# Kernel tuning notes

Hardware: AMD Instinct MI355X
Metric: run time of the kernel (lower is better)

The kernel has to match this reference:

```python
import jax, jax.numpy as jnp
import numpy as np

N_NODES = 20000
N_EDGES = 160000
N_GRAPHS = 64
IN_DIM = 1304  # 1280 + 24
NEG_SLOPE = 0.2


def gat_conv(x, src, dst, W, a_src, a_dst, b, heads, out_ch):
    """PyG-style GATConv (source_to_target flow, self loops already appended).
    x: [N, in], W: [in, heads*out], a_src/a_dst: [heads, out], b: [heads*out].
    Returns [N, heads*out] (concat=True)."""
    N = x.shape[0]
    h = (x @ W).reshape(N, heads, out_ch)                 # [N, H, C]
    e_src = jnp.sum(h * a_src[None], axis=-1)             # [N, H]
    e_dst = jnp.sum(h * a_dst[None], axis=-1)             # [N, H]
    e = jax.nn.leaky_relu(e_src[src] + e_dst[dst], NEG_SLOPE)  # [E, H]
    # softmax over incoming edges of each destination node
    e_max = jax.ops.segment_max(e, dst, num_segments=N)   # [N, H]
    e_exp = jnp.exp(e - e_max[dst])
    denom = jax.ops.segment_sum(e_exp, dst, num_segments=N)
    alpha = e_exp / (denom[dst] + 1e-16)                  # [E, H]
    msg = h[src] * alpha[:, :, None]                      # [E, H, C]
    out = jax.ops.segment_sum(msg, dst, num_segments=N)   # [N, H, C]
    return out.reshape(N, heads * out_ch) + b


def setup_inputs() -> dict:
    key = jax.random.key(0)
    ks = jax.random.split(key, 20)
    x = jax.random.normal(ks[0], (N_NODES, IN_DIM), dtype=jnp.float32)
    edge_index = jax.random.randint(ks[1], (2, N_EDGES), 0, N_NODES, dtype=jnp.int32)
    phy = jax.random.normal(ks[2], (N_GRAPHS, 188), dtype=jnp.float32)
    batch = jnp.sort(jax.random.randint(ks[3], (N_NODES,), 0, N_GRAPHS, dtype=jnp.int32))

    def glorot(k, shape):
        fan_in, fan_out = shape[0], shape[-1]
        lim = jnp.sqrt(6.0 / (fan_in + fan_out))
        return jax.random.uniform(k, shape, jnp.float32, -lim, lim)

    params = {
        # conv1: GATConv(1304, 256, heads=3)
        "W1": glorot(ks[4], (IN_DIM, 3 * 256)),
        "a_src1": glorot(ks[5], (3, 256)) * 0.1,
        "a_dst1": glorot(ks[6], (3, 256)) * 0.1,
        "b1": jnp.zeros((3 * 256,), jnp.float32),
        # conv2: GATConv(768, 256, heads=1)
        "W2": glorot(ks[7], (3 * 256, 256)),
        "a_src2": glorot(ks[8], (1, 256)) * 0.1,
        "a_dst2": glorot(ks[9], (1, 256)) * 0.1,
        "b2": jnp.zeros((256,), jnp.float32),
        # fc1
        "fc1_w1": glorot(ks[10], (188, 128)), "fc1_b1": jnp.zeros((128,), jnp.float32),
        "fc1_w2": glorot(ks[11], (128, 128)), "fc1_b2": jnp.zeros((128,), jnp.float32),
        # fc2
        "fc2_w1": glorot(ks[12], (256 + 128, 192)), "fc2_b1": jnp.zeros((192,), jnp.float32),
        "fc2_w2": glorot(ks[13], (192, 2)), "fc2_b2": jnp.zeros((2,), jnp.float32),
    }
    return {"x": x, "edge_index": edge_index, "phy": phy, "batch": batch, **params}


def reference(x, edge_index, phy, batch,
              W1, a_src1, a_dst1, b1,
              W2, a_src2, a_dst2, b2,
              fc1_w1, fc1_b1, fc1_w2, fc1_b2,
              fc2_w1, fc2_b1, fc2_w2, fc2_b2):
    N = x.shape[0]
    # add self loops (PyG GATConv default)
    loops = jnp.arange(N, dtype=edge_index.dtype)
    src = jnp.concatenate([edge_index[0], loops])
    dst = jnp.concatenate([edge_index[1], loops])

    h = gat_conv(x, src, dst, W1, a_src1, a_dst1, b1, heads=3, out_ch=256)
    h = jax.nn.relu(h)  # dropout is identity at inference
    h = gat_conv(h, src, dst, W2, a_src2, a_dst2, b2, heads=1, out_ch=256)

    # global mean pool per graph
    sums = jax.ops.segment_sum(h, batch, num_segments=N_GRAPHS)        # [B, 256]
    cnts = jax.ops.segment_sum(jnp.ones((N,), h.dtype), batch, num_segments=N_GRAPHS)
    pooled = sums / jnp.maximum(cnts, 1.0)[:, None]

    mid = jax.nn.relu(phy @ fc1_w1 + fc1_b1)
    mid = jax.nn.relu(mid @ fc1_w2 + fc1_b2)

    z = jnp.concatenate([pooled, mid], axis=1)                          # [B, 384]
    z = jax.nn.relu(z @ fc2_w1 + fc2_b1)
    logits = z @ fc2_w2 + fc2_b2
    return jax.nn.softmax(logits, axis=1)
```

## Files before the change

kernel.cpp:

```cpp
#include <hip/hip_runtime.h>
#include <hip/hip_bf16.h>
#include <math.h>

#define NN    20000
#define MP1   20224
#define NP    20096
#define E0    160000
#define EL    180000
#define NG    64
#define INDIM 1304
#define K1P   1344
#define GNT   21
#define GNX   3
#define GMB   79
#define NWG1  (GMB * GNX)
#define FB    19
#define NEG_SLOPE 0.2f
#define NSB   20
#define PCH   32

#define ZB    80
#define XB    13272
#define WB    4800

typedef __bf16 bf16x8 __attribute__((ext_vector_type(8)));
typedef __bf16 bf16x4 __attribute__((ext_vector_type(4)));
typedef float  f32x4  __attribute__((ext_vector_type(4)));

__device__ __forceinline__ void gload16(const void* g, void* l) {
    __builtin_amdgcn_global_load_lds(
        (const __attribute__((address_space(1))) void*)g,
        (__attribute__((address_space(3))) void*)l, 16, 0, 0);
}

#define BAR()  { __builtin_amdgcn_s_barrier(); asm volatile("" ::: "memory"); }
#define VMW(n) { asm volatile("s_waitcnt vmcnt(" #n ")" ::: "memory"); __builtin_amdgcn_sched_barrier(0); }

__global__ __launch_bounds__(256)
void init_kernel(uint4* __restrict__ zreg, int n16,
                 const float* __restrict__ X, __hip_bfloat16* __restrict__ Xb,
                 const float* __restrict__ W1, const float* __restrict__ W2,
                 __hip_bfloat16* __restrict__ w1t, __hip_bfloat16* __restrict__ w2t) {
    const int b = blockIdx.x, t = threadIdx.x;
    if (b < ZB) {
        int i = b * 256 + t;
        if (i < n16) zreg[i] = (uint4){0u, 0u, 0u, 0u};
        return;
    }
    if (b < ZB + XB) {
        int idx = (b - ZB) * 256 + t;
        const int nb = K1P / 8;
        int row = idx / nb;
        int cb = (idx - row * nb) * 8;
        union { __hip_bfloat16 h[8]; float4 f4; } u;
        if (row < NN && cb + 8 <= INDIM) {
            const float4* p = (const float4*)(X + (size_t)row * INDIM + cb);
            float4 u0 = p[0], u1 = p[1];
            u.h[0] = __float2bfloat16(u0.x); u.h[1] = __float2bfloat16(u0.y);
            u.h[2] = __float2bfloat16(u0.z); u.h[3] = __float2bfloat16(u0.w);
            u.h[4] = __float2bfloat16(u1.x); u.h[5] = __float2bfloat16(u1.y);
            u.h[6] = __float2bfloat16(u1.z); u.h[7] = __float2bfloat16(u1.w);
        } else {
#pragma unroll
            for (int e = 0; e < 8; e++) {
                float f = (row < NN && cb + e < INDIM) ? X[(size_t)row * INDIM + cb + e] : 0.f;
                u.h[e] = __float2bfloat16(f);
            }
        }
        *(float4*)(Xb + (size_t)row * K1P + cb) = u.f4;
        return;
    }
    {
        int idx = (b - ZB - XB) * 256 + t;
        const int n1 = 768 * K1P;
        if (idx < n1) {
            int n = idx / K1P, k = idx - n * K1P;
            float f = (k < INDIM) ? W1[(size_t)k * 768 + n] : 0.f;
            w1t[idx] = __float2bfloat16(f);
        } else {
            int i2 = idx - n1;
            if (i2 < 256 * 768) {
                int n = i2 / 768, k = i2 - n * 768;
                w2t[i2] = __float2bfloat16(W2[(size_t)k * 256 + n]);
            }
        }
    }
}

__device__ __forceinline__ void stA(const __hip_bfloat16* __restrict__ A, int bm, int kt, int mh,
                                    char* abuf, int w, int l) {
#pragma unroll
    for (int u = 0; u < 2; u++) {
        int rl = (w << 3) + (l >> 3);
        int lrow = u * 128 + mh * 64 + rl;
        int skb = ((l & 7) << 4) ^ ((rl & 7) << 4);
        const char* g = (const char*)(A + (size_t)(bm + lrow) * K1P + kt * 64) + skb;
        gload16(g, abuf + (u * 128 + mh * 64) * 128 + (w << 10));
    }
}

__device__ __forceinline__ void stB(const __hip_bfloat16* __restrict__ Bt, int bn, int kt, int nh,
                                    char* bbuf, int w, int l) {
#pragma unroll
    for (int u = 0; u < 2; u++) {
        int c = u * 2 + (w >> 2);
        int row0 = c * 64 + nh * 32;
        int rl = ((w & 3) << 3) + (l >> 3);
        int skb = ((l & 7) << 4) ^ ((rl & 7) << 4);
        const char* g = (const char*)(Bt + (size_t)(bn + row0 + rl) * K1P + kt * 64) + skb;
        gload16(g, bbuf + row0 * 128 + ((w & 3) << 10));
    }
}

__global__ __launch_bounds__(512)
void gemm256(const __hip_bfloat16* __restrict__ A,
             const __hip_bfloat16* __restrict__ Bt,
             __hip_bfloat16* __restrict__ C,
             const float* __restrict__ a_src, const float* __restrict__ a_dst,
             float* __restrict__ esrc, float* __restrict__ edst, int M,
             const int* __restrict__ ei, const int* __restrict__ off,
             int* __restrict__ cur, int* __restrict__ csr) {
    __shared__ char lds[65536];
    const int t = threadIdx.x;

    if (blockIdx.x >= NWG1) {
        for (int e = (blockIdx.x - NWG1) * 512 + t; e < EL; e += FB * 512) {
            int d = (e < E0) ? ei[E0 + e] : (e - E0);
            int s = (e < E0) ? ei[e] : (e - E0);
            int pos = off[d] + atomicAdd(&cur[d], 1);
            csr[pos] = s;
        }
        return;
    }

    const int w = t >> 6, l = t & 63;
    const int wm = w >> 2, wn = w & 3;
    const int fr = l & 15, fq = l >> 4;
    const int amask = (fr & 7) << 4;

    const int nwg = NWG1;
    const int q8 = nwg >> 3, r8 = nwg & 7;
    const int xcd = blockIdx.x & 7, sub = blockIdx.x >> 3;
    const int logical = (xcd < r8 ? xcd * (q8 + 1) : r8 * (q8 + 1) + (xcd - r8) * q8) + sub;
    const int bm = (logical / GNX) * 256;
    const int bn = (logical % GNX) * 256;

    f32x4 acc[8][4];
#pragma unroll
    for (int i = 0; i < 8; i++)
#pragma unroll
        for (int j = 0; j < 4; j++) acc[i][j] = (f32x4){0.f, 0.f, 0.f, 0.f};

    char* Ab = lds;
    char* Bb = lds + 32768;

    stA(A, bm, 0, 0, Ab, w, l);
    stB(Bt, bn, 0, 0, Bb, w, l);
    stB(Bt, bn, 0, 1, Bb, w, l);
    stA(A, bm, 0, 1, Ab, w, l);

    for (int kt = 0; kt < GNT; kt++) {
        const bool nl = (kt + 1 < GNT);
        bf16x8 a_c[4][2], b_c0[2][2], b_c1[2][2];

        VMW(4);
        BAR();
#pragma unroll
        for (int im = 0; im < 4; im++)
#pragma unroll
            for (int kk = 0; kk < 2; kk++)
                a_c[im][kk] = *(const bf16x8*)(Ab + (wm * 128 + im * 16 + fr) * 128 + ((kk * 64 + fq * 16) ^ amask));
#pragma unroll
        for (int jn = 0; jn < 2; jn++)
#pragma unroll
            for (int kk = 0; kk < 2; kk++)
                b_c0[jn][kk] = *(const bf16x8*)(Bb + (wn * 64 + jn * 16 + fr) * 128 + ((kk * 64 + fq * 16) ^ amask));
        if (nl) stA(A, bm, kt + 1, 0, Ab, w, l);
        __builtin_amdgcn_s_setprio(1);
#pragma unroll
        for (int im = 0; im < 4; im++)
#pragma unroll
            for (int jn = 0; jn < 2; jn++)
#pragma unroll
                for (int kk = 0; kk < 2; kk++)
                    acc[im][jn] = __builtin_amdgcn_mfma_f32_16x16x32_bf16(a_c[im][kk], b_c0[jn][kk], acc[im][jn], 0, 0, 0);
        __builtin_amdgcn_s_setprio(0);

        if (nl) { VMW(4); } else { VMW(2); }
        BAR();
#pragma unroll
        for (int jn = 0; jn < 2; jn++)
#pragma unroll
            for (int kk = 0; kk < 2; kk++)
                b_c1[jn][kk] = *(const bf16x8*)(Bb + (wn * 64 + 32 + jn * 16 + fr) * 128 + ((kk * 64 + fq * 16) ^ amask));
        if (nl) stB(Bt, bn, kt + 1, 0, Bb, w, l);
        __builtin_amdgcn_s_setprio(1);
#pragma unroll
        for (int im = 0; im < 4; im++)
#pragma unroll
            for (int jn = 0; jn < 2; jn++)
#pragma unroll
                for (int kk = 0; kk < 2; kk++)
                    acc[im][2 + jn] = __builtin_amdgcn_mfma_f32_16x16x32_bf16(a_c[im][kk], b_c1[jn][kk], acc[im][2 + jn], 0, 0, 0);
        __builtin_amdgcn_s_setprio(0);

        if (nl) { VMW(4); } else { VMW(0); }
        BAR();
#pragma unroll
        for (int im = 0; im < 4; im++)
#pragma unroll
            for (int kk = 0; kk < 2; kk++)
                a_c[im][kk] = *(const bf16x8*)(Ab + (wm * 128 + 64 + im * 16 + fr) * 128 + ((kk * 64 + fq * 16) ^ amask));
        if (nl) stB(Bt, bn, kt + 1, 1, Bb, w, l);
        __builtin_amdgcn_s_setprio(1);
#pragma unroll
        for (int im = 0; im < 4; im++)
#pragma unroll
            for (int jn = 0; jn < 2; jn++)
#pragma unroll
                for (int kk = 0; kk < 2; kk++)
                    acc[4 + im][jn] = __builtin_amdgcn_mfma_f32_16x16x32_bf16(a_c[im][kk], b_c0[jn][kk], acc[4 + im][jn], 0, 0, 0);
        __builtin_amdgcn_s_setprio(0);

        if (nl) stA(A, bm, kt + 1, 1, Ab, w, l);
        __builtin_amdgcn_s_setprio(1);
#pragma unroll
        for (int im = 0; im < 4; im++)
#pragma unroll
            for (int jn = 0; jn < 2; jn++)
#pragma unroll
                for (int kk = 0; kk < 2; kk++)
                    acc[4 + im][2 + jn] = __builtin_amdgcn_mfma_f32_16x16x32_bf16(a_c[im][kk], b_c1[jn][kk], acc[4 + im][2 + jn], 0, 0, 0);
        __builtin_amdgcn_s_setprio(0);
    }

#pragma unroll
    for (int i = 0; i < 8; i++)
#pragma unroll
        for (int j = 0; j < 4; j++)
#pragma unroll
            for (int r = 0; r < 4; r++) {
                int row = bm + wm * 128 + i * 16 + fq * 4 + r;
                int col = bn + wn * 64 + j * 16 + fr;
                if (row < M) C[(size_t)row * 768 + col] = __float2bfloat16(acc[i][j][r]);
            }

    const int head = bn >> 8;
    float asv[4], adv[4];
#pragma unroll
    for (int j = 0; j < 4; j++) {
        asv[j] = a_src[head * 256 + wn * 64 + j * 16 + fr];
        adv[j] = a_dst[head * 256 + wn * 64 + j * 16 + fr];
    }
    __syncthreads();
    float* eb = (float*)lds;
#pragma unroll
    for (int i = 0; i < 8; i++) {
#pragma unroll
        for (int r = 0; r < 4; r++) {
            float ps = 0.f, pd = 0.f;
#pragma unroll
            for (int j = 0; j < 4; j++) { ps += acc[i][j][r] * asv[j]; pd += acc[i][j][r] * adv[j]; }
#pragma unroll
            for (int o = 8; o >= 1; o >>= 1) { ps += __shfl_xor(ps, o, 64); pd += __shfl_xor(pd, o, 64); }
            if (fr == 0) {
                int rowl = wm * 128 + i * 16 + fq * 4 + r;
                eb[(rowl * 4 + wn) * 2 + 0] = ps;
                eb[(rowl * 4 + wn) * 2 + 1] = pd;
            }
        }
    }
    __syncthreads();
    if (t < 256) {
        int row = bm + t;
        if (row < M) {
            float s = eb[t * 8 + 0] + eb[t * 8 + 2] + eb[t * 8 + 4] + eb[t * 8 + 6];
            float d = eb[t * 8 + 1] + eb[t * 8 + 3] + eb[t * 8 + 5] + eb[t * 8 + 7];
            esrc[row * 3 + head] = s;
            edst[row * 3 + head] = d;
        }
    }
}

__global__ __launch_bounds__(256)
void gemm2_fused(const __hip_bfloat16* __restrict__ A,
                 const __hip_bfloat16* __restrict__ Bt,
                 __hip_bfloat16* __restrict__ C,
                 const float* __restrict__ a_src2, const float* __restrict__ a_dst2,
                 float* __restrict__ esrc, float* __restrict__ edst,
                 int M, int N, int K, int NX) {
    __shared__ __hip_bfloat16 As[2][128 * 32];
    __shared__ __hip_bfloat16 Bs[2][128 * 32];
    const int t = threadIdx.x;
    const int w = t >> 6;
    const int l = t & 63;

    const int nwg = gridDim.x;
    const int q = nwg >> 3, r = nwg & 7;
    const int xcd = blockIdx.x & 7, idx = blockIdx.x >> 3;
    const int logical = (xcd < r ? xcd * (q + 1) : r * (q + 1) + (xcd - r) * q) + idx;
    const int bm = (logical / NX) * 128;
    const int bn = (logical % NX) * 128;

    const int wm = (w >> 1) * 64;
    const int wn = (w & 1) * 64;

    f32x4 acc[4][4];
#pragma unroll
    for (int i = 0; i < 4; i++)
#pragma unroll
        for (int j = 0; j < 4; j++) acc[i][j] = (f32x4){0.f, 0.f, 0.f, 0.f};

    const int sr = t >> 2;
    const int sc = (t & 3) * 8;
    const __hip_bfloat16* a0 = A  + (size_t)(bm + sr)      * K + sc;
    const __hip_bfloat16* a1 = A  + (size_t)(bm + 64 + sr) * K + sc;
    const __hip_bfloat16* b0 = Bt + (size_t)(bn + sr)      * K + sc;
    const __hip_bfloat16* b1 = Bt + (size_t)(bn + 64 + sr) * K + sc;

    const int fr = l & 15;
    const int fq = l >> 4;
    const int NT = K / 32;

    auto stage = [&](int k0, int b) {
        char* asb = (char*)&As[b][0];
        char* bsb = (char*)&Bs[b][0];
        gload16(a0 + k0, asb + w * 1024);
        gload16(a1 + k0, asb + 4096 + w * 1024);
        gload16(b0 + k0, bsb + w * 1024);
        gload16(b1 + k0, bsb + 4096 + w * 1024);
    };

    stage(0, 0);
    __syncthreads();

    for (int kt = 0; kt < NT; kt++) {
        const int cb = kt & 1;
        if (kt + 1 < NT) stage((kt + 1) * 32, cb ^ 1);
        bf16x8 av[4], bv[4];
#pragma unroll
        for (int i = 0; i < 4; i++)
            av[i] = *(const bf16x8*)&As[cb][(wm + i * 16 + fr) * 32 + fq * 8];
#pragma unroll
        for (int j = 0; j < 4; j++)
            bv[j] = *(const bf16x8*)&Bs[cb][(wn + j * 16 + fr) * 32 + fq * 8];
#pragma unroll
        for (int i = 0; i < 4; i++)
#pragma unroll
            for (int j = 0; j < 4; j++)
                acc[i][j] = __builtin_amdgcn_mfma_f32_16x16x32_bf16(av[i], bv[j], acc[i][j], 0, 0, 0);
        __syncthreads();
    }

#pragma unroll
    for (int i = 0; i < 4; i++) {
#pragma unroll
        for (int j = 0; j < 4; j++) {
#pragma unroll
            for (int r2 = 0; r2 < 4; r2++) {
                int row = bm + wm + i * 16 + fq * 4 + r2;
                int col = bn + wn + j * 16 + fr;
                if (row < M) C[(size_t)row * N + col] = __float2bfloat16(acc[i][j][r2]);
            }
        }
    }

    float asv[4], adv[4];
#pragma unroll
    for (int j = 0; j < 4; j++) {
        asv[j] = a_src2[bn + wn + j * 16 + fr];
        adv[j] = a_dst2[bn + wn + j * 16 + fr];
    }
    __syncthreads();
    float* eb = (float*)&As[0][0];
#pragma unroll
    for (int i = 0; i < 4; i++) {
#pragma unroll
        for (int r2 = 0; r2 < 4; r2++) {
            float ps = 0.f, pd = 0.f;
#pragma unroll
            for (int j = 0; j < 4; j++) { ps += acc[i][j][r2] * asv[j]; pd += acc[i][j][r2] * adv[j]; }
#pragma unroll
            for (int o = 8; o >= 1; o >>= 1) { ps += __shfl_xor(ps, o, 64); pd += __shfl_xor(pd, o, 64); }
            if (fr == 0) {
                int rowl = wm + i * 16 + fq * 4 + r2;
                int wnIdx = wn >> 6;
                eb[(rowl * 2 + wnIdx) * 2 + 0] = ps;
                eb[(rowl * 2 + wnIdx) * 2 + 1] = pd;
            }
        }
    }
    __syncthreads();
    if (t < 128) {
        int row = bm + t;
        if (row < M) {
            atomicAdd(&esrc[row], eb[t * 4 + 0] + eb[t * 4 + 2]);
            atomicAdd(&edst[row], eb[t * 4 + 1] + eb[t * 4 + 3]);
        }
    }
}

__global__ void hist_kernel(const int* __restrict__ ei, int* __restrict__ deg) {
    int e = blockIdx.x * 256 + threadIdx.x;
    if (e >= EL) return;
    int d = (e < E0) ? ei[E0 + e] : (e - E0);
    atomicAdd(&deg[d], 1);
}

__global__ __launch_bounds__(1024)
void scan_blk(const int* __restrict__ deg, int* __restrict__ off, int* __restrict__ bsum) {
    __shared__ int wsum[16];
    const int b = blockIdx.x, t = threadIdx.x, lane = t & 63, wv = t >> 6;
    const int i = b * 1024 + t;
    int v = (i < NN) ? deg[i] : 0;
    int x = v;
#pragma unroll
    for (int o = 1; o < 64; o <<= 1) {
        int y = __shfl_up(x, o, 64);
        if (lane >= o) x += y;
    }
    if (lane == 63) wsum[wv] = x;
    __syncthreads();
    if (wv == 0 && lane < 16) {
        int s = wsum[lane];
#pragma unroll
        for (int o = 1; o < 16; o <<= 1) {
            int y = __shfl_up(s, o, 64);
            if (lane >= o) s += y;
        }
        wsum[lane] = s;
    }
    __syncthreads();
    int woff = (wv == 0) ? 0 : wsum[wv - 1];
    if (i < NN) off[i + 1] = woff + x;
    if (t == 1023) bsum[b] = wsum[15];
}

__global__ __launch_bounds__(1024)
void scan_add(int* __restrict__ off, const int* __restrict__ bsum) {
    __shared__ int boffs[NSB];
    const int b = blockIdx.x, t = threadIdx.x;
    if (t < 64) {
        int lane = t;
        int v = (lane < NSB) ? bsum[lane] : 0;
        int x = v;
#pragma unroll
        for (int o = 1; o < 64; o <<= 1) {
            int y = __shfl_up(x, o, 64);
            if (lane >= o) x += y;
        }
        if (lane < NSB) boffs[lane] = x - v;
    }
    __syncthreads();
    const int i = b * 1024 + t;
    if (i < NN) off[i + 1] += boffs[b];
    if (b == 0 && t == 0) off[0] = 0;
}

template<int H, bool RELU, typename OutT>
__global__ __launch_bounds__(256)
void gat_aggregate(const __hip_bfloat16* __restrict__ hfeat,
                   const float* __restrict__ esrc,
                   const float* __restrict__ edst,
                   const int* __restrict__ off, const int* __restrict__ csr,
                   const float* __restrict__ bias,
                   OutT* __restrict__ out, int N) {
    const int wv = threadIdx.x >> 6, lane = threadIdx.x & 63;
    const int pair = blockIdx.x * 4 + wv;
    if (pair >= N * H) return;
    const int n = pair / H;
    const int h = pair - n * H;
    const int beg = off[n];
    const int deg = off[n + 1] - beg;

    const float ed = edst[n * H + h];
    float m = -INFINITY, den = 0.f;
    f32x4 acc = (f32x4){0.f, 0.f, 0.f, 0.f};

    for (int base = 0; base < deg; base += 64) {
        const int i = base + lane;
        int s = 0;
        float lg = -INFINITY;
        if (i < deg) {
            s = csr[beg + i];
            float v = esrc[s * H + h] + ed;
            lg = (v >= 0.f) ? v : NEG_SLOPE * v;
        }
        float cm = lg;
#pragma unroll
        for (int o = 1; o < 64; o <<= 1)
            cm = fmaxf(cm, __shfl_xor(cm, o, 64));
        float nm = fmaxf(m, cm);
        float sc = expf(m - nm);
        den *= sc;
#pragma unroll
        for (int e = 0; e < 4; e++) acc[e] *= sc;
        m = nm;
        float wgt = (i < deg) ? expf(lg - m) : 0.f;
        den += wgt;
        const int cnt = min(64, deg - base);
        for (int j = 0; j < cnt; j++) {
            int sj = __shfl(s, j, 64);
            float wj = __shfl(wgt, j, 64);
            bf16x4 hv = *(const bf16x4*)(hfeat + (size_t)sj * (H * 256) + h * 256 + 4 * lane);
#pragma unroll
            for (int e = 0; e < 4; e++) acc[e] += wj * (float)hv[e];
        }
    }
#pragma unroll
    for (int o = 1; o < 64; o <<= 1) den += __shfl_xor(den, o, 64);

    float inv = 1.f / (den + 1e-16f);
    if constexpr (sizeof(OutT) == 2) {
        bf16x4 r;
#pragma unroll
        for (int e = 0; e < 4; e++) {
            float f = acc[e] * inv + bias[h * 256 + 4 * lane + e];
            if (RELU) f = fmaxf(f, 0.f);
            r[e] = (__bf16)f;
        }
        *(bf16x4*)((__hip_bfloat16*)out + (size_t)n * (H * 256) + h * 256 + 4 * lane) = r;
    } else {
        float4 r;
        float* rp = &r.x;
#pragma unroll
        for (int e = 0; e < 4; e++) {
            float f = acc[e] * inv + bias[h * 256 + 4 * lane + e];
            if (RELU) f = fmaxf(f, 0.f);
            rp[e] = f;
        }
        *(float4*)((float*)out + (size_t)n * (H * 256) + h * 256 + 4 * lane) = r;
    }
}

__device__ __forceinline__ int lower_bound_batch(const int* __restrict__ batch, int key) {
    int lo = 0, hi = NN;
    while (lo < hi) {
        int mid = (lo + hi) >> 1;
        if (batch[mid] < key) lo = mid + 1; else hi = mid;
    }
    return lo;
}

__global__ __launch_bounds__(256)
void pool_partial(const __hip_bfloat16* __restrict__ out2, const int* __restrict__ batch,
                  float* __restrict__ partial, float* __restrict__ cnts) {
    const int g = blockIdx.x, c = blockIdx.y, t = threadIdx.x;
    const int s = lower_bound_batch(batch, g);
    const int e = lower_bound_batch(batch, g + 1);
    float a0 = 0.f, a1 = 0.f, a2 = 0.f, a3 = 0.f;
    int n = s + c;
    for (; n + 3 * PCH < e; n += 4 * PCH) {
        float v0 = __bfloat162float(out2[(size_t)n * 256 + t]);
        float v1 = __bfloat162float(out2[(size_t)(n + PCH) * 256 + t]);
        float v2 = __bfloat162float(out2[(size_t)(n + 2 * PCH) * 256 + t]);
        float v3 = __bfloat162float(out2[(size_t)(n + 3 * PCH) * 256 + t]);
        a0 += v0; a1 += v1; a2 += v2; a3 += v3;
    }
    for (; n < e; n += PCH) a0 += __bfloat162float(out2[(size_t)n * 256 + t]);
    partial[((size_t)g * PCH + c) * 256 + t] = a0 + a1 + a2 + a3;
    if (t == 0 && c == 0) cnts[g] = (float)(e - s);
}

__global__ __launch_bounds__(256)
void head_kernel(const float* __restrict__ partial, const float* __restrict__ cnts,
                 const float* __restrict__ phy,
                 const float* __restrict__ w11, const float* __restrict__ b11,
                 const float* __restrict__ w12, const float* __restrict__ b12,
                 const float* __restrict__ w21, const float* __restrict__ b21,
                 const float* __restrict__ w22, const float* __restrict__ b22,
                 float* __restrict__ out) {
    int g = blockIdx.x, t = threadIdx.x;
    __shared__ float ph[188];
    __shared__ float z[384];
    __shared__ float mid[128];
    __shared__ float t1[192];
    __shared__ float lg[2];
    if (t < 188) ph[t] = phy[g * 188 + t];
    {
        float s = 0.f;
#pragma unroll
        for (int c = 0; c < PCH; c++) s += partial[((size_t)g * PCH + c) * 256 + t];
        z[t] = s / fmaxf(cnts[g], 1.0f);
    }
    __syncthreads();
    if (t < 128) {
        float sm = b11[t];
        for (int k = 0; k < 188; k++) sm += ph[k] * w11[k * 128 + t];
        mid[t] = fmaxf(sm, 0.f);
    }
    __syncthreads();
    if (t < 128) {
        float sm = b12[t];
        for (int k = 0; k < 128; k++) sm += mid[k] * w12[k * 128 + t];
        z[256 + t] = fmaxf(sm, 0.f);
    }
    __syncthreads();
    if (t < 192) {
        float sm = b21[t];
        for (int k = 0; k < 384; k++) sm += z[k] * w21[k * 192 + t];
        t1[t] = fmaxf(sm, 0.f);
    }
    __syncthreads();
    if (t < 2) {
        float sm = b22[t];
        for (int k = 0; k < 192; k++) sm += t1[k] * w22[k * 2 + t];
        lg[t] = sm;
    }
    __syncthreads();
    if (t == 0) {
        float mx = fmaxf(lg[0], lg[1]);
        float e0 = expf(lg[0] - mx), e1 = expf(lg[1] - mx);
        float d = e0 + e1;
        out[g * 2 + 0] = e0 / d;
        out[g * 2 + 1] = e1 / d;
    }
}

extern "C" void kernel_launch(void* const* d_in, const int* in_sizes, int n_in,
                              void* d_out, int out_size, void* d_ws, size_t ws_size,
                              hipStream_t stream) {
    const float* x       = (const float*)d_in[0];
    const int*   ei      = (const int*)  d_in[1];
    const float* phy     = (const float*)d_in[2];
    const int*   batch   = (const int*)  d_in[3];
    const float* W1      = (const float*)d_in[4];
    const float* a_src1  = (const float*)d_in[5];
    const float* a_dst1  = (const float*)d_in[6];
    const float* b1      = (const float*)d_in[7];
    const float* W2      = (const float*)d_in[8];
    const float* a_src2  = (const float*)d_in[9];
    const float* a_dst2  = (const float*)d_in[10];
    const float* b2      = (const float*)d_in[11];
    const float* fc1_w1  = (const float*)d_in[12];
    const float* fc1_b1  = (const float*)d_in[13];
    const float* fc1_w2  = (const float*)d_in[14];
    const float* fc1_b2  = (const float*)d_in[15];
    const float* fc2_w1  = (const float*)d_in[16];
    const float* fc2_b1  = (const float*)d_in[17];
    const float* fc2_w2  = (const float*)d_in[18];
    const float* fc2_b2  = (const float*)d_in[19];
    float* out = (float*)d_out;

    char* base = (char*)d_ws;
    size_t o = 0;
    auto alloc = [&](size_t bytes) { size_t r = o; o += (bytes + 255) & ~255ULL; return r; };

    size_t o_xb   = alloc((size_t)MP1 * K1P * 2);
    size_t o_w1t  = alloc((size_t)768 * K1P * 2);
    size_t o_w2t  = alloc((size_t)256 * 768 * 2);
    size_t o_h1b  = alloc((size_t)NP * 768 * 2);
    size_t o_hob  = alloc((size_t)NP * 768 * 2);
    size_t o_es1  = alloc((size_t)NN * 3 * 4);
    size_t o_ed1  = alloc((size_t)NN * 3 * 4);
    size_t o_es2  = alloc((size_t)NN * 4);
    size_t o_ed2  = alloc((size_t)NN * 4);
    size_t o_deg  = alloc((size_t)(NN + 1) * 4);
    size_t o_cur  = alloc((size_t)NN * 4);
    size_t o_zend = o;
    size_t o_off  = alloc((size_t)(NN + 1) * 4);
    size_t o_csr  = alloc((size_t)EL * 4);
    size_t o_bsum = alloc((size_t)NSB * 4);
    size_t o_part = alloc((size_t)NG * PCH * 256 * 4);
    size_t o_cnts = alloc((size_t)NG * 4);

    __hip_bfloat16* xb   = (__hip_bfloat16*)(base + o_xb);
    __hip_bfloat16* w1t  = (__hip_bfloat16*)(base + o_w1t);
    __hip_bfloat16* w2t  = (__hip_bfloat16*)(base + o_w2t);
    __hip_bfloat16* h1b  = (__hip_bfloat16*)(base + o_h1b);
    __hip_bfloat16* hob  = (__hip_bfloat16*)(base + o_hob);
    __hip_bfloat16* h2b  = (__hip_bfloat16*)(base + o_xb);
    __hip_bfloat16* out2 = (__hip_bfloat16*)(base + o_xb + (size_t)24 * 1024 * 1024);
    float* es1   = (float*)(base + o_es1);
    float* ed1   = (float*)(base + o_ed1);
    float* es2   = (float*)(base + o_es2);
    float* ed2   = (float*)(base + o_ed2);
    int*   deg   = (int*)(base + o_deg);
    int*   cur   = (int*)(base + o_cur);
    int*   offs  = (int*)(base + o_off);
    int*   csr   = (int*)(base + o_csr);
    int*   bsum  = (int*)(base + o_bsum);
    float* part  = (float*)(base + o_part);
    float* cnts  = (float*)(base + o_cnts);

    {
        int n16 = (int)((o_zend - o_es2) / 16);
        init_kernel<<<ZB + XB + WB, 256, 0, stream>>>((uint4*)(base + o_es2), n16,
                                                      x, xb, W1, W2, w1t, w2t);
    }

    hist_kernel<<<(EL + 255) / 256, 256, 0, stream>>>(ei, deg);
    scan_blk<<<NSB, 1024, 0, stream>>>(deg, offs, bsum);
    scan_add<<<NSB, 1024, 0, stream>>>(offs, bsum);

    gemm256<<<NWG1 + FB, 512, 0, stream>>>(xb, w1t, h1b, a_src1, a_dst1, es1, ed1, NN,
                                           ei, offs, cur, csr);
    gat_aggregate<3, true, __hip_bfloat16><<<(NN * 3 + 3) / 4, 256, 0, stream>>>(h1b, es1, ed1, offs, csr, b1, hob, NN);

    gemm2_fused<<<2 * 157, 256, 0, stream>>>(hob, w2t, h2b, a_src2, a_dst2, es2, ed2, NN, 256, 768, 2);
    gat_aggregate<1, false, __hip_bfloat16><<<(NN + 3) / 4, 256, 0, stream>>>(h2b, es2, ed2, offs, csr, b2, out2, NN);

    pool_partial<<<dim3(NG, PCH), 256, 0, stream>>>(out2, batch, part, cnts);
    head_kernel<<<NG, 256, 0, stream>>>(part, cnts, phy,
                                        fc1_w1, fc1_b1, fc1_w2, fc1_b2,
                                        fc2_w1, fc2_b1, fc2_w2, fc2_b2, out);
}
```

Measured before the change: 230.3 us.

## Fuse fp32-to-bf16 conversion of X into GEMM A-tile loading

Drops the separate pass that converted X to a padded bf16 copy in init_kernel. The first GEMM now reads fp32 X directly into registers, converts to bf16 and writes swizzled tiles into LDS, with reworked vmcnt/lgkmcnt waits to keep the loads overlapped. This removes a full write and re-read of the converted matrix (about 54 MB of traffic). In exchange each A tile pulls twice the bytes from global memory, and the register staging can cost registers or weaken latency hiding in the main loop.

```diff
diff --git a/kernel.cpp b/kernel.cpp
--- a/kernel.cpp
+++ b/kernel.cpp
@@ -3,12 +3,12 @@
 #include <math.h>
 
 #define NN    20000
-#define MP1   20224
 #define NP    20096
 #define E0    160000
 #define EL    180000
 #define NG    64
 #define INDIM 1304
+#define NG8   (INDIM / 8)
 #define K1P   1344
 #define GNT   21
 #define GNX   3
@@ -20,7 +20,6 @@
 #define PCH   32
 
 #define ZB    80
-#define XB    13272
 #define WB    4800
 
 typedef __bf16 bf16x8 __attribute__((ext_vector_type(8)));
@@ -35,10 +34,10 @@
 
 #define BAR()  { __builtin_amdgcn_s_barrier(); asm volatile("" ::: "memory"); }
 #define VMW(n) { asm volatile("s_waitcnt vmcnt(" #n ")" ::: "memory"); __builtin_amdgcn_sched_barrier(0); }
+#define LGW()  { asm volatile("s_waitcnt lgkmcnt(0)" ::: "memory"); __builtin_amdgcn_sched_barrier(0); }
 
 __global__ __launch_bounds__(256)
 void init_kernel(uint4* __restrict__ zreg, int n16,
-                 const float* __restrict__ X, __hip_bfloat16* __restrict__ Xb,
                  const float* __restrict__ W1, const float* __restrict__ W2,
                  __hip_bfloat16* __restrict__ w1t, __hip_bfloat16* __restrict__ w2t) {
     const int b = blockIdx.x, t = threadIdx.x;
@@ -47,31 +46,8 @@
         if (i < n16) zreg[i] = (uint4){0u, 0u, 0u, 0u};
         return;
     }
-    if (b < ZB + XB) {
+    {
         int idx = (b - ZB) * 256 + t;
-        const int nb = K1P / 8;
-        int row = idx / nb;
-        int cb = (idx - row * nb) * 8;
-        union { __hip_bfloat16 h[8]; float4 f4; } u;
-        if (row < NN && cb + 8 <= INDIM) {
-            const float4* p = (const float4*)(X + (size_t)row * INDIM + cb);
-            float4 u0 = p[0], u1 = p[1];
-            u.h[0] = __float2bfloat16(u0.x); u.h[1] = __float2bfloat16(u0.y);
-            u.h[2] = __float2bfloat16(u0.z); u.h[3] = __float2bfloat16(u0.w);
-            u.h[4] = __float2bfloat16(u1.x); u.h[5] = __float2bfloat16(u1.y);
-            u.h[6] = __float2bfloat16(u1.z); u.h[7] = __float2bfloat16(u1.w);
-        } else {
-#pragma unroll
-            for (int e = 0; e < 8; e++) {
-                float f = (row < NN && cb + e < INDIM) ? X[(size_t)row * INDIM + cb + e] : 0.f;
-                u.h[e] = __float2bfloat16(f);
-            }
-        }
-        *(float4*)(Xb + (size_t)row * K1P + cb) = u.f4;
-        return;
-    }
-    {
-        int idx = (b - ZB - XB) * 256 + t;
         const int n1 = 768 * K1P;
         if (idx < n1) {
             int n = idx / K1P, k = idx - n * K1P;
@@ -87,15 +63,34 @@
     }
 }
 
-__device__ __forceinline__ void stA(const __hip_bfloat16* __restrict__ A, int bm, int kt, int mh,
-                                    char* abuf, int w, int l) {
+__device__ __forceinline__ void aLoad(const float* __restrict__ X, int bm, int kt, int mh,
+                                      int w, int l, float4 (&v)[2][2]) {
+    const int g8 = min(kt * 8 + (l & 7), NG8 - 1);
+    const int rl = (w << 3) + (l >> 3);
 #pragma unroll
     for (int u = 0; u < 2; u++) {
-        int rl = (w << 3) + (l >> 3);
         int lrow = u * 128 + mh * 64 + rl;
-        int skb = ((l & 7) << 4) ^ ((rl & 7) << 4);
-        const char* g = (const char*)(A + (size_t)(bm + lrow) * K1P + kt * 64) + skb;
-        gload16(g, abuf + (u * 128 + mh * 64) * 128 + (w << 10));
+        int row = min(bm + lrow, NN - 1);
+        const float4* p = (const float4*)(X + (size_t)row * INDIM + g8 * 8);
+        v[u][0] = p[0];
+        v[u][1] = p[1];
+    }
+}
+
+__device__ __forceinline__ void aWrite(char* abuf, int bm, int kt, int mh, int w, int l,
+                                       const float4 (&v)[2][2]) {
+    const bool cok = (kt * 8 + (l & 7)) < NG8;
+    const int rl = (w << 3) + (l >> 3);
+#pragma unroll
+    for (int u = 0; u < 2; u++) {
+        int lrow = u * 128 + mh * 64 + rl;
+        bool ok = cok && (bm + lrow < NN);
+        union { __hip_bfloat16 h[8]; bf16x8 vv; } uu;
+        const float* f = (const float*)&v[u][0];
+#pragma unroll
+        for (int e = 0; e < 8; e++) uu.h[e] = __float2bfloat16(ok ? f[e] : 0.f);
+        int byte = lrow * 128 + ((((l & 7) << 4)) ^ ((rl & 7) << 4));
+        *(bf16x8*)(abuf + byte) = uu.vv;
     }
 }
 
@@ -113,7 +108,7 @@
 }
 
 __global__ __launch_bounds__(512)
-void gemm256(const __hip_bfloat16* __restrict__ A,
+void gemm256(const float* __restrict__ X,
              const __hip_bfloat16* __restrict__ Bt,
              __hip_bfloat16* __restrict__ C,
              const float* __restrict__ a_src, const float* __restrict__ a_dst,
@@ -154,16 +149,21 @@
     char* Ab = lds;
     char* Bb = lds + 32768;
 
-    stA(A, bm, 0, 0, Ab, w, l);
+    float4 av0[2][2], av1[2][2];
+
+    aLoad(X, bm, 0, 0, w, l, av0);
+    aLoad(X, bm, 0, 1, w, l, av1);
     stB(Bt, bn, 0, 0, Bb, w, l);
     stB(Bt, bn, 0, 1, Bb, w, l);
-    stA(A, bm, 0, 1, Ab, w, l);
+    VMW(8); aWrite(Ab, bm, 0, 0, w, l, av0);
+    VMW(4); aWrite(Ab, bm, 0, 1, w, l, av1);
+    LGW();
 
     for (int kt = 0; kt < GNT; kt++) {
         const bool nl = (kt + 1 < GNT);
         bf16x8 a_c[4][2], b_c0[2][2], b_c1[2][2];
 
-        VMW(4);
+        if (kt == 0) { VMW(2); } else { VMW(6); }
         BAR();
 #pragma unroll
         for (int im = 0; im < 4; im++)
@@ -175,7 +175,9 @@
 #pragma unroll
             for (int kk = 0; kk < 2; kk++)
                 b_c0[jn][kk] = *(const bf16x8*)(Bb + (wn * 64 + jn * 16 + fr) * 128 + ((kk * 64 + fq * 16) ^ amask));
-        if (nl) stA(A, bm, kt + 1, 0, Ab, w, l);
+        if (nl) aLoad(X, bm, kt + 1, 0, w, l, av0);
+        if (nl) { VMW(4); } else { VMW(0); }
+        if (kt > 0) aWrite(Ab, bm, kt, 1, w, l, av1);
         __builtin_amdgcn_s_setprio(1);
 #pragma unroll
         for (int im = 0; im < 4; im++)
@@ -185,15 +187,19 @@
                 for (int kk = 0; kk < 2; kk++)
                     acc[im][jn] = __builtin_amdgcn_mfma_f32_16x16x32_bf16(a_c[im][kk], b_c0[jn][kk], acc[im][jn], 0, 0, 0);
         __builtin_amdgcn_s_setprio(0);
-
-        if (nl) { VMW(4); } else { VMW(2); }
+        LGW();
+
         BAR();
 #pragma unroll
         for (int jn = 0; jn < 2; jn++)
 #pragma unroll
             for (int kk = 0; kk < 2; kk++)
                 b_c1[jn][kk] = *(const bf16x8*)(Bb + (wn * 64 + 32 + jn * 16 + fr) * 128 + ((kk * 64 + fq * 16) ^ amask));
-        if (nl) stB(Bt, bn, kt + 1, 0, Bb, w, l);
+        if (nl) {
+            stB(Bt, bn, kt + 1, 0, Bb, w, l);
+            VMW(2);
+            aWrite(Ab, bm, kt + 1, 0, w, l, av0);
+        }
         __builtin_amdgcn_s_setprio(1);
 #pragma unroll
         for (int im = 0; im < 4; im++)
@@ -203,8 +209,8 @@
                 for (int kk = 0; kk < 2; kk++)
                     acc[im][2 + jn] = __builtin_amdgcn_mfma_f32_16x16x32_bf16(a_c[im][kk], b_c1[jn][kk], acc[im][2 + jn], 0, 0, 0);
         __builtin_amdgcn_s_setprio(0);
-
-        if (nl) { VMW(4); } else { VMW(0); }
+        LGW();
+
         BAR();
 #pragma unroll
         for (int im = 0; im < 4; im++)
@@ -222,7 +228,7 @@
                     acc[4 + im][jn] = __builtin_amdgcn_mfma_f32_16x16x32_bf16(a_c[im][kk], b_c0[jn][kk], acc[4 + im][jn], 0, 0, 0);
         __builtin_amdgcn_s_setprio(0);
 
-        if (nl) stA(A, bm, kt + 1, 1, Ab, w, l);
+        if (nl) aLoad(X, bm, kt + 1, 1, w, l, av1);
         __builtin_amdgcn_s_setprio(1);
 #pragma unroll
         for (int im = 0; im < 4; im++)
@@ -646,7 +652,7 @@
     size_t o = 0;
     auto alloc = [&](size_t bytes) { size_t r = o; o += (bytes + 255) & ~255ULL; return r; };
 
-    size_t o_xb   = alloc((size_t)MP1 * K1P * 2);
+    size_t o_scr  = alloc((size_t)48 * 1024 * 1024);
     size_t o_w1t  = alloc((size_t)768 * K1P * 2);
     size_t o_w2t  = alloc((size_t)256 * 768 * 2);
     size_t o_h1b  = alloc((size_t)NP * 768 * 2);
@@ -664,13 +670,12 @@
     size_t o_part = alloc((size_t)NG * PCH * 256 * 4);
     size_t o_cnts = alloc((size_t)NG * 4);
 
-    __hip_bfloat16* xb   = (__hip_bfloat16*)(base + o_xb);
     __hip_bfloat16* w1t  = (__hip_bfloat16*)(base + o_w1t);
     __hip_bfloat16* w2t  = (__hip_bfloat16*)(base + o_w2t);
     __hip_bfloat16* h1b  = (__hip_bfloat16*)(base + o_h1b);
     __hip_bfloat16* hob  = (__hip_bfloat16*)(base + o_hob);
-    __hip_bfloat16* h2b  = (__hip_bfloat16*)(base + o_xb);
-    __hip_bfloat16* out2 = (__hip_bfloat16*)(base + o_xb + (size_t)24 * 1024 * 1024);
+    __hip_bfloat16* h2b  = (__hip_bfloat16*)(base + o_scr);
+    __hip_bfloat16* out2 = (__hip_bfloat16*)(base + o_scr + (size_t)24 * 1024 * 1024);
     float* es1   = (float*)(base + o_es1);
     float* ed1   = (float*)(base + o_ed1);
     float* es2   = (float*)(base + o_es2);
@@ -685,15 +690,15 @@
 
     {
         int n16 = (int)((o_zend - o_es2) / 16);
-        init_kernel<<<ZB + XB + WB, 256, 0, stream>>>((uint4*)(base + o_es2), n16,
-                                                      x, xb, W1, W2, w1t, w2t);
+        init_kernel<<<ZB + WB, 256, 0, stream>>>((uint4*)(base + o_es2), n16,
+                                                 W1, W2, w1t, w2t);
     }
 
     hist_kernel<<<(EL + 255) / 256, 256, 0, stream>>>(ei, deg);
     scan_blk<<<NSB, 1024, 0, stream>>>(deg, offs, bsum);
     scan_add<<<NSB, 1024, 0, stream>>>(offs, bsum);
 
-    gemm256<<<NWG1 + FB, 512, 0, stream>>>(xb, w1t, h1b, a_src1, a_dst1, es1, ed1, NN,
+    gemm256<<<NWG1 + FB, 512, 0, stream>>>(x, w1t, h1b, a_src1, a_dst1, es1, ed1, NN,
                                            ei, offs, cur, csr);
     gat_aggregate<3, true, __hip_bfloat16><<<(NN * 3 + 3) / 4, 256, 0, stream>>>(h1b, es1, ed1, offs, csr, b1, hob, NN);
 
```

After: 237.4 us. 3.1% more time.
